# Kernel optimization log

Hardware: AMD Instinct MI355X
Metric: run time of the kernel (lower is better)

The kernel has to match this reference:

```python
import jax, jax.numpy as jnp
import numpy as np

B, N, M = 8, 4096, 4096
CHAMFER_W, EMD_W, UNC_W = 1.0, 0.5, 0.01


def setup_inputs() -> dict:
    key = jax.random.key(0)
    k1, k2, k3 = jax.random.split(key, 3)
    return {
        "pred_pc": jax.random.normal(k1, (B, N, 3), dtype=jnp.float32),
        "target_pc": jax.random.normal(k2, (B, M, 3), dtype=jnp.float32),
        "uncertainty": jax.random.uniform(k3, (B, N), dtype=jnp.float32),
    }


def reference(pred_pc, target_pc, uncertainty):
    # squared pairwise distances via ||p||^2 + ||t||^2 - 2 p.t  -> [B, N, M]
    pred_sq = jnp.sum(pred_pc ** 2, axis=2, keepdims=True)            # [B, N, 1]
    tgt_sq = jnp.sum(target_pc ** 2, axis=2, keepdims=True)           # [B, M, 1]
    cross = jnp.einsum('bnd,bmd->bnm', pred_pc, target_pc)            # [B, N, M]
    d2 = pred_sq + jnp.swapaxes(tgt_sq, 1, 2) - 2.0 * cross           # [B, N, M]

    # ChamferDistanceLoss: mean of min squared dists both directions
    chamfer = jnp.mean(jnp.min(d2, axis=2)) + jnp.mean(jnp.min(d2, axis=1))

    # EMDLoss: torch.cdist p=2 (euclidean), min over targets, mean
    dist = jnp.sqrt(jnp.clip(d2, 0.0))
    emd = jnp.mean(jnp.min(dist, axis=2))

    # uncertainty regularizer
    unc_reg = jnp.mean(uncertainty) * UNC_W

    total = chamfer * CHAMFER_W + emd * EMD_W + unc_reg
    return total
```

## Files before the change

### kernel.cpp

```cpp
#include <hip/hip_runtime.h>
#include <math.h>

typedef _Float16 half8 __attribute__((ext_vector_type(8)));
typedef float    f32x4 __attribute__((ext_vector_type(4)));

#define Bb 8
#define Nn 4096
#define Mm 4096
#define BLOCK 512
#define WAVES 8
#define QB 256
#define NTW 2
#define MTILES (Mm / 16)
#define GRID 256

__global__ void __launch_bounds__(BLOCK) chamfer_fused_kernel(
    const float* __restrict__ pred,
    const float* __restrict__ targ,
    const float* __restrict__ unc,
    float4* __restrict__ psum,
    unsigned* __restrict__ counter,
    float* __restrict__ out)
{
    __shared__ uint4 fragB[Mm];
    float* wsum = (float*)fragB;

    const int tid  = threadIdx.x;
    const int lane = tid & 63;
    const int wave = tid >> 6;

    const int id  = blockIdx.x;
    const int qt  = id & 15;
    const int b   = (id >> 4) & 7;
    const int dir = id >> 7;

    const float* Q = dir ? targ : pred;
    const float* T = dir ? pred : targ;

    float su = 0.f;
    if (tid < 32) {
        float4 uu = ((const float4*)unc)[id * 32 + tid];
        su = (uu.x + uu.y) + (uu.z + uu.w);
    }

    for (int s = tid; s < Mm; s += BLOCK) {
        const float* g = T + ((size_t)b * Mm + s) * 3;
        _Float16 xh = (_Float16)g[0], yh = (_Float16)g[1], zh = (_Float16)g[2];
        float xq = (float)xh, yq = (float)yh, zq = (float)zh;
        float tt = fmaf(xq, xq, fmaf(yq, yq, zq * zq));
        _Float16 th = (_Float16)tt;
        _Float16 tl = (_Float16)(tt - (float)th);
        const _Float16 m2 = (_Float16)(-2.0f);
        half8 h;
        h[0] = m2 * xh; h[1] = m2 * yh; h[2] = m2 * zh; h[3] = (_Float16)1.0f;
        h[4] = th; h[5] = (_Float16)1.0f; h[6] = tl; h[7] = (_Float16)0.0f;
        fragB[s] = *reinterpret_cast<uint4*>(&h);
    }

    const bool lo16 = (lane < 16);
    half8 a[NTW];
    #pragma unroll
    for (int t = 0; t < NTW; ++t) {
        half8 h;
        #pragma unroll
        for (int e = 0; e < 8; ++e) h[e] = (_Float16)0.0f;
        if (lo16) {
            const int n = qt * QB + (wave * NTW + t) * 16 + lane;
            const float* g = Q + ((size_t)b * Nn + n) * 3;
            _Float16 xh = (_Float16)g[0], yh = (_Float16)g[1], zh = (_Float16)g[2];
            float xq = (float)xh, yq = (float)yh, zq = (float)zh;
            float pp = fmaf(xq, xq, fmaf(yq, yq, zq * zq));
            _Float16 ph = (_Float16)pp;
            _Float16 pl = (_Float16)(pp - (float)ph);
            h[0] = xh; h[1] = yh; h[2] = zh; h[3] = ph;
            h[4] = (_Float16)1.0f; h[5] = pl; h[6] = (_Float16)1.0f; h[7] = (_Float16)0.0f;
        }
        a[t] = h;
    }
    __syncthreads();

    const int col = lane & 15;
    const f32x4 cz = {0.f, 0.f, 0.f, 0.f};
    const float inf = __builtin_inff();
    f32x4 acc0 = {inf, inf, inf, inf}, acc1 = acc0;
    #pragma unroll 4
    for (int j = 0; j < MTILES; j += 2) {
        half8 b0 = *reinterpret_cast<const half8*>(&fragB[(j << 4) + col]);
        half8 b1 = *reinterpret_cast<const half8*>(&fragB[((j + 1) << 4) + col]);
        f32x4 c00 = __builtin_amdgcn_mfma_f32_16x16x32_f16(a[0], b0, cz, 0, 0, 0);
        f32x4 c01 = __builtin_amdgcn_mfma_f32_16x16x32_f16(a[0], b1, cz, 0, 0, 0);
        f32x4 c10 = __builtin_amdgcn_mfma_f32_16x16x32_f16(a[1], b0, cz, 0, 0, 0);
        f32x4 c11 = __builtin_amdgcn_mfma_f32_16x16x32_f16(a[1], b1, cz, 0, 0, 0);
        #pragma unroll
        for (int k = 0; k < 4; ++k) {
            acc0[k] = fminf(fminf(acc0[k], c00[k]), c01[k]);
            acc1[k] = fminf(fminf(acc1[k], c10[k]), c11[k]);
        }
    }

    float s1 = 0.f, s2 = 0.f;
    #pragma unroll
    for (int t = 0; t < NTW; ++t) {
        f32x4 v = t ? acc1 : acc0;
        #pragma unroll
        for (int m = 1; m < 16; m <<= 1) {
            #pragma unroll
            for (int k = 0; k < 4; ++k)
                v[k] = fminf(v[k], __shfl_xor(v[k], m));
        }
        if (col == 0) {
            #pragma unroll
            for (int k = 0; k < 4; ++k) {
                const float d2 = v[k];
                s1 += d2;
                s2 += sqrtf(fmaxf(d2, 0.f));
            }
        }
    }
    #pragma unroll
    for (int m = 1; m < 64; m <<= 1) {
        s1 += __shfl_xor(s1, m);
        s2 += __shfl_xor(s2, m);
        su += __shfl_xor(su, m);
    }

    __syncthreads();
    if (lane == 0) {
        wsum[wave * 4 + 0] = s1;
        wsum[wave * 4 + 1] = s2;
        wsum[wave * 4 + 2] = su;
    }
    __syncthreads();
    if (tid == 0) {
        float S1 = 0.f, S2 = 0.f, SU = 0.f;
        #pragma unroll
        for (int w = 0; w < WAVES; ++w) {
            S1 += wsum[w * 4 + 0]; S2 += wsum[w * 4 + 1]; SU += wsum[w * 4 + 2];
        }
        psum[id] = make_float4(S1, S2, SU, 0.f);
        __threadfence();
        unsigned old = atomicAdd(counter, 1u);
        ((int*)wsum)[32] = (((old + 1) & (GRID - 1)) == 0) ? 1 : 0;
    }
    __syncthreads();
    if (((int*)wsum)[32]) {
        __threadfence();
        float sa = 0.f, sb = 0.f, se = 0.f, sU = 0.f;
        if (tid < GRID) {
            float4 v = psum[tid];
            if (tid < GRID / 2) { sa = v.x; se = v.y; }
            else                { sb = v.x; }
            sU = v.z;
        }
        #pragma unroll
        for (int m = 1; m < 64; m <<= 1) {
            sa += __shfl_xor(sa, m); sb += __shfl_xor(sb, m);
            se += __shfl_xor(se, m); sU += __shfl_xor(sU, m);
        }
        __syncthreads();
        if (lane == 0) {
            wsum[wave * 4 + 0] = sa; wsum[wave * 4 + 1] = sb;
            wsum[wave * 4 + 2] = se; wsum[wave * 4 + 3] = sU;
        }
        __syncthreads();
        if (tid == 0) {
            float SA = 0.f, SB = 0.f, SE = 0.f, SU2 = 0.f;
            #pragma unroll
            for (int w = 0; w < WAVES; ++w) {
                SA += wsum[w * 4 + 0]; SB += wsum[w * 4 + 1];
                SE += wsum[w * 4 + 2]; SU2 += wsum[w * 4 + 3];
            }
            const float invBN = 1.0f / (float)(Bb * Nn);
            const float invBM = 1.0f / (float)(Bb * Mm);
            out[0] = (SA * invBN + SB * invBM) + 0.5f * (SE * invBN)
                   + 0.01f * (SU2 * invBN);
        }
    }
}

extern "C" void kernel_launch(void* const* d_in, const int* in_sizes, int n_in,
                              void* d_out, int out_size, void* d_ws, size_t ws_size,
                              hipStream_t stream) {
    const float* pred = (const float*)d_in[0];
    const float* targ = (const float*)d_in[1];
    const float* unc  = (const float*)d_in[2];
    float* out = (float*)d_out;

    float4*   psum    = (float4*)d_ws;
    unsigned* counter = (unsigned*)((char*)d_ws + 4096);

    chamfer_fused_kernel<<<GRID, BLOCK, 0, stream>>>(pred, targ, unc,
                                                     psum, counter, out);
}
```

Before: 26.35 us.

## Split target range across waves with 8 query tiles per wave and LDS min merge

Each wave now holds 8 query A-fragments and sweeps only a quarter of the target tiles, so every B-fragment loaded from LDS feeds 8 MFMAs instead of 2. Partial minima from the four waves sharing a query group are merged through shared memory. The 16-lane column reduction now uses DPP row operations instead of shuffles. The cost is more accumulator registers (8 f32x4) and an extra LDS merge pass with barriers.

```diff
diff --git a/kernel.cpp b/kernel.cpp
--- a/kernel.cpp
+++ b/kernel.cpp
@@ -10,9 +10,22 @@
 #define BLOCK 512
 #define WAVES 8
 #define QB 256
-#define NTW 2
-#define MTILES (Mm / 16)
+#define NTA 8
 #define GRID 256
+
+template<int CTRL>
+__device__ __forceinline__ float dppmin(float v) {
+    int iv = __float_as_int(v);
+    iv = __builtin_amdgcn_update_dpp(iv, iv, CTRL, 0xF, 0xF, false);
+    return fminf(v, __int_as_float(iv));
+}
+__device__ __forceinline__ float colmin16(float v) {
+    v = dppmin<0xB1>(v);
+    v = dppmin<0x4E>(v);
+    v = dppmin<0x141>(v);
+    v = dppmin<0x140>(v);
+    return v;
+}
 
 __global__ void __launch_bounds__(BLOCK) chamfer_fused_kernel(
     const float* __restrict__ pred,
@@ -23,11 +36,14 @@
     float* __restrict__ out)
 {
     __shared__ uint4 fragB[Mm];
-    float* wsum = (float*)fragB;
+    float* smin = (float*)fragB;
+    float* wsum = smin + 1024;
 
     const int tid  = threadIdx.x;
     const int lane = tid & 63;
     const int wave = tid >> 6;
+    const int g     = wave >> 2;
+    const int wslot = wave & 3;
 
     const int id  = blockIdx.x;
     const int qt  = id & 15;
@@ -44,8 +60,8 @@
     }
 
     for (int s = tid; s < Mm; s += BLOCK) {
-        const float* g = T + ((size_t)b * Mm + s) * 3;
-        _Float16 xh = (_Float16)g[0], yh = (_Float16)g[1], zh = (_Float16)g[2];
+        const float* gp = T + ((size_t)b * Mm + s) * 3;
+        _Float16 xh = (_Float16)gp[0], yh = (_Float16)gp[1], zh = (_Float16)gp[2];
         float xq = (float)xh, yq = (float)yh, zq = (float)zh;
         float tt = fmaf(xq, xq, fmaf(yq, yq, zq * zq));
         _Float16 th = (_Float16)tt;
@@ -57,17 +73,16 @@
         fragB[s] = *reinterpret_cast<uint4*>(&h);
     }
 
-    const bool lo16 = (lane < 16);
-    half8 a[NTW];
-    #pragma unroll
-    for (int t = 0; t < NTW; ++t) {
+    half8 a[NTA];
+    #pragma unroll
+    for (int t = 0; t < NTA; ++t) {
         half8 h;
         #pragma unroll
         for (int e = 0; e < 8; ++e) h[e] = (_Float16)0.0f;
-        if (lo16) {
-            const int n = qt * QB + (wave * NTW + t) * 16 + lane;
-            const float* g = Q + ((size_t)b * Nn + n) * 3;
-            _Float16 xh = (_Float16)g[0], yh = (_Float16)g[1], zh = (_Float16)g[2];
+        if (lane < 16) {
+            const int n = qt * QB + g * 128 + t * 16 + lane;
+            const float* gp = Q + ((size_t)b * Nn + n) * 3;
+            _Float16 xh = (_Float16)gp[0], yh = (_Float16)gp[1], zh = (_Float16)gp[2];
             float xq = (float)xh, yq = (float)yh, zq = (float)zh;
             float pp = fmaf(xq, xq, fmaf(yq, yq, zq * zq));
             _Float16 ph = (_Float16)pp;
@@ -82,40 +97,49 @@
     const int col = lane & 15;
     const f32x4 cz = {0.f, 0.f, 0.f, 0.f};
     const float inf = __builtin_inff();
-    f32x4 acc0 = {inf, inf, inf, inf}, acc1 = acc0;
-    #pragma unroll 4
-    for (int j = 0; j < MTILES; j += 2) {
+    f32x4 acc[NTA];
+    #pragma unroll
+    for (int t = 0; t < NTA; ++t) { acc[t][0] = inf; acc[t][1] = inf; acc[t][2] = inf; acc[t][3] = inf; }
+
+    const int jbase = wslot * 64;
+    #pragma unroll 2
+    for (int jj = 0; jj < 64; jj += 2) {
+        const int j = jbase + jj;
         half8 b0 = *reinterpret_cast<const half8*>(&fragB[(j << 4) + col]);
         half8 b1 = *reinterpret_cast<const half8*>(&fragB[((j + 1) << 4) + col]);
-        f32x4 c00 = __builtin_amdgcn_mfma_f32_16x16x32_f16(a[0], b0, cz, 0, 0, 0);
-        f32x4 c01 = __builtin_amdgcn_mfma_f32_16x16x32_f16(a[0], b1, cz, 0, 0, 0);
-        f32x4 c10 = __builtin_amdgcn_mfma_f32_16x16x32_f16(a[1], b0, cz, 0, 0, 0);
-        f32x4 c11 = __builtin_amdgcn_mfma_f32_16x16x32_f16(a[1], b1, cz, 0, 0, 0);
-        #pragma unroll
-        for (int k = 0; k < 4; ++k) {
-            acc0[k] = fminf(fminf(acc0[k], c00[k]), c01[k]);
-            acc1[k] = fminf(fminf(acc1[k], c10[k]), c11[k]);
-        }
-    }
-
-    float s1 = 0.f, s2 = 0.f;
-    #pragma unroll
-    for (int t = 0; t < NTW; ++t) {
-        f32x4 v = t ? acc1 : acc0;
-        #pragma unroll
-        for (int m = 1; m < 16; m <<= 1) {
+        #pragma unroll
+        for (int t = 0; t < NTA; ++t) {
+            f32x4 c = __builtin_amdgcn_mfma_f32_16x16x32_f16(a[t], b0, cz, 0, 0, 0);
+            f32x4 d = __builtin_amdgcn_mfma_f32_16x16x32_f16(a[t], b1, cz, 0, 0, 0);
             #pragma unroll
             for (int k = 0; k < 4; ++k)
-                v[k] = fminf(v[k], __shfl_xor(v[k], m));
-        }
+                acc[t][k] = fminf(fminf(acc[t][k], c[k]), d[k]);
+        }
+    }
+
+    __syncthreads();
+    #pragma unroll
+    for (int t = 0; t < NTA; ++t) {
+        float v0 = colmin16(acc[t][0]);
+        float v1 = colmin16(acc[t][1]);
+        float v2 = colmin16(acc[t][2]);
+        float v3 = colmin16(acc[t][3]);
         if (col == 0) {
-            #pragma unroll
-            for (int k = 0; k < 4; ++k) {
-                const float d2 = v[k];
-                s1 += d2;
-                s2 += sqrtf(fmaxf(d2, 0.f));
-            }
-        }
+            const int qloc = g * 128 + t * 16 + (lane >> 4) * 4;
+            smin[(qloc + 0) * 4 + wslot] = v0;
+            smin[(qloc + 1) * 4 + wslot] = v1;
+            smin[(qloc + 2) * 4 + wslot] = v2;
+            smin[(qloc + 3) * 4 + wslot] = v3;
+        }
+    }
+    __syncthreads();
+
+    float s1 = 0.f, s2 = 0.f;
+    if (tid < QB) {
+        float4 mv = ((const float4*)smin)[tid];
+        float d2 = fminf(fminf(mv.x, mv.y), fminf(mv.z, mv.w));
+        s1 = d2;
+        s2 = sqrtf(fmaxf(d2, 0.f));
     }
     #pragma unroll
     for (int m = 1; m < 64; m <<= 1) {
@@ -123,7 +147,6 @@
         s2 += __shfl_xor(s2, m);
         su += __shfl_xor(su, m);
     }
-
     __syncthreads();
     if (lane == 0) {
         wsum[wave * 4 + 0] = s1;
```

Measured after the change: 27.43 us. 1.04x slower.
